# Kernel optimization log

Measured on AMD Instinct MI355X. Metric: run time of the kernel, lower is better.

Reference implementation:

```python
import math
import jax, jax.numpy as jnp
import numpy as np

B, T, D = 4, 2048, 1024
H = 16
DK = D // H


def setup_inputs() -> dict:
    key = jax.random.key(0)
    ks = jax.random.split(key, 9)
    s = 1.0 / math.sqrt(D)
    return {
        "x": jax.random.normal(ks[0], (B, T, D), dtype=jnp.float32),
        "Wq": jax.random.normal(ks[1], (D, D), dtype=jnp.float32) * s,
        "bq": jax.random.normal(ks[2], (D,), dtype=jnp.float32) * s,
        "Wk": jax.random.normal(ks[3], (D, D), dtype=jnp.float32) * s,
        "bk": jax.random.normal(ks[4], (D,), dtype=jnp.float32) * s,
        "Wv": jax.random.normal(ks[5], (D, D), dtype=jnp.float32) * s,
        "bv": jax.random.normal(ks[6], (D,), dtype=jnp.float32) * s,
        "Wo": jax.random.normal(ks[7], (D, D), dtype=jnp.float32) * s,
        "bo": jax.random.normal(ks[8], (D,), dtype=jnp.float32) * s,
    }


def reference(x, Wq, bq, Wk, bk, Wv, bv, Wo, bo):
    Bx, Tx, C = x.shape
    # projections -> [B, H, T, d_k]
    q = (x @ Wq + bq).reshape(Bx, Tx, H, DK).transpose(0, 2, 1, 3)
    k = (x @ Wk + bk).reshape(Bx, Tx, H, DK).transpose(0, 2, 1, 3)
    v = (x @ Wv + bv).reshape(Bx, Tx, H, DK).transpose(0, 2, 1, 3)
    # scores [B, H, T, T], scaled
    scores = jnp.einsum("bhqd,bhkd->bhqk", q, k) / math.sqrt(DK)
    causal = jnp.tril(jnp.ones((Tx, Tx), dtype=bool))
    scores = jnp.where(causal[None, None, :, :], scores, -jnp.inf)
    attn = jax.nn.softmax(scores, axis=-1)  # dropout p=0.0 (eval)
    out = jnp.einsum("bhqk,bhkd->bhqd", attn, v)
    out = out.transpose(0, 2, 1, 3).reshape(Bx, Tx, C)
    return out @ Wo + bo
```

## Files before the change

kernel.cpp:

```cpp
#include <hip/hip_runtime.h>
#include <stdint.h>
#include <math.h>

typedef __attribute__((ext_vector_type(8))) __bf16 bf16x8;
typedef __attribute__((ext_vector_type(4))) __bf16 bf16x4;
typedef __attribute__((ext_vector_type(4))) float f32x4;
typedef __attribute__((ext_vector_type(4))) short short4v;

__device__ __forceinline__ void load_lds16(const void* g, void* l) {
  __builtin_amdgcn_global_load_lds((__attribute__((address_space(1))) void*)(g),
                                   (__attribute__((address_space(3))) void*)(l),
                                   16, 0, 0);
}

__device__ __forceinline__ uint32_t pack_bf2(float a, float b) {
  union { __bf16 h; uint16_t u; } x, y;
  x.h = (__bf16)a; y.h = (__bf16)b;
  return (uint32_t)x.u | ((uint32_t)y.u << 16);
}

__device__ __forceinline__ short4v mk4(uint32_t lo, uint32_t hi) {
  union { uint32_t d[2]; short4v v; } u;
  u.d[0] = lo; u.d[1] = hi;
  return u.v;
}

__device__ __forceinline__ f32x4 mfma16(short4v a, short4v b, f32x4 c) {
#if defined(__has_builtin) && __has_builtin(__builtin_amdgcn_mfma_f32_16x16x16bf16_1k)
  return __builtin_amdgcn_mfma_f32_16x16x16bf16_1k(a, b, c, 0, 0, 0);
#else
  asm volatile("v_mfma_f32_16x16x16_bf16 %0, %1, %2, %0"
               : "+v"(c) : "v"(a), "v"(b));
  return c;
#endif
}

__global__ __launch_bounds__(256)
void convert_x(const float* __restrict__ xf, __bf16* __restrict__ xb) {
  const size_t i = ((size_t)blockIdx.x * 256 + threadIdx.x) * 8;
  const float4 u0 = *(const float4*)(xf + i);
  const float4 u1 = *(const float4*)(xf + i + 4);
  bf16x8 v;
  v[0] = (__bf16)u0.x; v[1] = (__bf16)u0.y; v[2] = (__bf16)u0.z; v[3] = (__bf16)u0.w;
  v[4] = (__bf16)u1.x; v[5] = (__bf16)u1.y; v[6] = (__bf16)u1.z; v[7] = (__bf16)u1.w;
  *(bf16x8*)&xb[i] = v;
}

__global__ __launch_bounds__(256)
void prep_weights(const float* __restrict__ Wq, const float* __restrict__ Wk,
                  const float* __restrict__ Wv, const float* __restrict__ Wo,
                  const float* __restrict__ bq, const float* __restrict__ bk,
                  const float* __restrict__ bv, const float* __restrict__ bo,
                  __bf16* __restrict__ Bt1, __bf16* __restrict__ Bt2,
                  float* __restrict__ bqkv, float* __restrict__ bo_f) {
  const int m = blockIdx.z;
  const float* W = (m == 0) ? Wq : (m == 1) ? Wk : (m == 2) ? Wv : Wo;
  __bf16* Out = (m == 3) ? Bt2 : Bt1 + (size_t)m * 1024 * 1024;
  const int kt = blockIdx.x * 64, nt = blockIdx.y * 64;
  __shared__ __bf16 tile[64 * 68];
  const int t = threadIdx.x;
#pragma unroll
  for (int i = 0; i < 16; i++) {
    int e = i * 256 + t;
    int r = e >> 6, c = e & 63;
    tile[r * 68 + c] = (__bf16)W[(size_t)(kt + r) * 1024 + nt + c];
  }
  __syncthreads();
#pragma unroll
  for (int i = 0; i < 16; i++) {
    int e = i * 256 + t;
    int r = e >> 6, c = e & 63;
    Out[(size_t)(nt + r) * 1024 + kt + c] = tile[c * 68 + r];
  }
  if (blockIdx.x == 0 && blockIdx.y == 0) {
    if (m < 3) {
      const float* bsrc = (m == 0) ? bq : (m == 1) ? bk : bv;
      for (int i = t; i < 1024; i += 256) bqkv[m * 1024 + i] = bsrc[i];
    } else {
      for (int i = t; i < 1024; i += 256) bo_f[i] = bo[i];
    }
  }
}

__global__ __launch_bounds__(256)
void gemm_bt(const __bf16* __restrict__ A, const __bf16* __restrict__ Bt,
             const float* __restrict__ bias, void* __restrict__ Cv,
             int out_f32, int M, int N, int K) {
  __shared__ __align__(16) __bf16 As[128 * 32];
  __shared__ __align__(16) __bf16 Bs[128 * 32];
  const int t = threadIdx.x;
  const int lane = t & 63;
  const int wave = t >> 6;
  const int bm = blockIdx.x * 128;
  const int bn = blockIdx.y * 128;
  const int wm = (wave >> 1) * 64;
  const int wn = (wave & 1) * 64;
  const int fm = lane & 15, fk = (lane >> 4) * 8;
  f32x4 acc[4][4] = {};

  const int r0 = t >> 2, kc = (t & 3) * 8;
  const __bf16* Ag0 = A + (size_t)(bm + r0) * K + kc;
  const __bf16* Ag1 = A + (size_t)(bm + 64 + r0) * K + kc;
  const __bf16* Bg0 = Bt + (size_t)(bn + r0) * K + kc;
  const __bf16* Bg1 = Bt + (size_t)(bn + 64 + r0) * K + kc;

  for (int k0 = 0; k0 < K; k0 += 32) {
    load_lds16(Ag0 + k0, &As[t * 8]);
    load_lds16(Ag1 + k0, &As[2048 + t * 8]);
    load_lds16(Bg0 + k0, &Bs[t * 8]);
    load_lds16(Bg1 + k0, &Bs[2048 + t * 8]);
    asm volatile("s_waitcnt vmcnt(0)" ::: "memory");
    __syncthreads();
    bf16x8 af[4], bfr[4];
#pragma unroll
    for (int i = 0; i < 4; i++) {
      af[i] = *(const bf16x8*)&As[(wm + i * 16 + fm) * 32 + fk];
      bfr[i] = *(const bf16x8*)&Bs[(wn + i * 16 + fm) * 32 + fk];
    }
#pragma unroll
    for (int i = 0; i < 4; i++)
#pragma unroll
      for (int j = 0; j < 4; j++)
        acc[i][j] = __builtin_amdgcn_mfma_f32_16x16x32_bf16(af[i], bfr[j], acc[i][j], 0, 0, 0);
    __syncthreads();
  }

  const int cm = (lane >> 4) * 4, cn = lane & 15;
#pragma unroll
  for (int i = 0; i < 4; i++)
#pragma unroll
    for (int j = 0; j < 4; j++) {
      const int col = bn + wn + j * 16 + cn;
      const float bvv = bias[col];
#pragma unroll
      for (int r = 0; r < 4; r++) {
        const int row = bm + wm + i * 16 + cm + r;
        const float val = acc[i][j][r] + bvv;
        if (out_f32) ((float*)Cv)[(size_t)row * N + col] = val;
        else ((__bf16*)Cv)[(size_t)row * N + col] = (__bf16)val;
      }
    }
}

__global__ __launch_bounds__(256)
void transpose_v(const __bf16* __restrict__ QKV, __bf16* __restrict__ Vt) {
  const int tt = blockIdx.x;
  const int bh = blockIdx.y;
  const int b = bh >> 4, h = bh & 15;
  __shared__ __bf16 tile[64 * 68];
  const int t = threadIdx.x;
#pragma unroll
  for (int i = 0; i < 16; i++) {
    int e = i * 256 + t;
    int tok = e >> 6, dk = e & 63;
    tile[tok * 68 + dk] =
        QKV[((size_t)b * 2048 + tt * 64 + tok) * 3072 + 2048 + h * 64 + dk];
  }
  __syncthreads();
#pragma unroll
  for (int i = 0; i < 16; i++) {
    int e = i * 256 + t;
    int dk = e >> 6, tok = e & 63;
    Vt[((size_t)bh * 64 + dk) * 2048 + tt * 64 + tok] = tile[tok * 68 + dk];
  }
}

__global__ __launch_bounds__(256)
void flash_attn(const __bf16* __restrict__ QKV, const __bf16* __restrict__ Vt,
                __bf16* __restrict__ O) {
  const int y = blockIdx.y;
  const int g = y >> 2, iy = y & 3;
  const int qt = (g == 0) ? (15 - iy)
               : (g == 1) ? iy
               : (g == 2) ? (7 - iy)
                          : (8 + iy);
  const int bh = blockIdx.x;
  const int b = bh >> 4, h = bh & 15;
  __shared__ __align__(16) __bf16 Ks[2][64 * 64];
  __shared__ __align__(16) __bf16 Vs[2][64 * 64];
  const int t = threadIdx.x, lane = t & 63, wave = t >> 6;
  const int fm = lane & 15, fq = lane >> 4;
  const int tok0 = t >> 3;
  const int csw = ((t & 7) ^ (tok0 & 7)) << 3;
  const int swb = (fm & 7) << 4;
  const int rb0 = (((fq << 4)) ^ swb) >> 1;
  const int rb1 = ((64 + (fq << 4)) ^ swb) >> 1;
  int voff[4];
#pragma unroll
  for (int nt = 0; nt < 4; nt++)
    voff[nt] = (((((nt << 1) | (fq >> 1))) ^ (fm & 7)) << 3) | ((fq & 1) << 2);

  const size_t kbase = ((size_t)b * 2048) * 3072 + 1024 + h * 64;
  const size_t vbase = (size_t)bh * 64 * 2048;
  const int nkt = 2 * qt + 2;
  const int qw = qt * 128 + wave * 32;
  const int qmax_w = qw + 31;
  const float SC = 0.18033688011112042f;
  const float THR_RAW = 44.3614195558365f;

  bf16x8 qf[2][2];
#pragma unroll
  for (int mi = 0; mi < 2; mi++) {
    const size_t qrow = ((size_t)b * 2048 + qw + mi * 16 + fm) * 3072 + h * 64;
    qf[mi][0] = *(const bf16x8*)&QKV[qrow + fq * 8];
    qf[mi][1] = *(const bf16x8*)&QKV[qrow + 32 + fq * 8];
  }

  const short4v ones4 = {(short)0x3F80, (short)0x3F80, (short)0x3F80, (short)0x3F80};

  f32x4 o_acc[2][4] = {};
  float m_i[2] = {-1e30f, -1e30f}, l_i[2] = {0.f, 0.f};

#define STAGE(KT, BUF)                                                          \
  {                                                                             \
    const int kb2 = (KT) * 64;                                                  \
    load_lds16(&QKV[kbase + (size_t)(kb2 + tok0) * 3072 + csw],                 \
               &Ks[BUF][t * 8]);                                                \
    load_lds16(&QKV[kbase + (size_t)(kb2 + 32 + tok0) * 3072 + csw],            \
               &Ks[BUF][2048 + t * 8]);                                         \
    load_lds16(&Vt[vbase + (size_t)tok0 * 2048 + kb2 + csw],                    \
               &Vs[BUF][t * 8]);                                                \
    load_lds16(&Vt[vbase + (size_t)(tok0 + 32) * 2048 + kb2 + csw],             \
               &Vs[BUF][2048 + t * 8]);                                         \
  }

  STAGE(0, 0);
  __syncthreads();
  int cur = 0;

  for (int kt = 0; kt < nkt; kt++) {
    const int kb = kt * 64;
    if (kt + 1 < nkt) STAGE(kt + 1, cur ^ 1);

    if (kb <= qmax_w) {
      const __bf16* Kc = Ks[cur];
      const __bf16* Vc = Vs[cur];

      f32x4 s[2][4];
      __builtin_amdgcn_s_setprio(1);
#pragma unroll
      for (int nt = 0; nt < 4; nt++) {
        const bf16x8 kf0 = *(const bf16x8*)&Kc[(nt * 16 + fm) * 64 + rb0];
        const bf16x8 kf1 = *(const bf16x8*)&Kc[(nt * 16 + fm) * 64 + rb1];
#pragma unroll
        for (int mi = 0; mi < 2; mi++) {
          f32x4 z = {};
          z = __builtin_amdgcn_mfma_f32_16x16x32_bf16(kf0, qf[mi][0], z, 0, 0, 0);
          z = __builtin_amdgcn_mfma_f32_16x16x32_bf16(kf1, qf[mi][1], z, 0, 0, 0);
          s[mi][nt] = z;
        }
      }
      __builtin_amdgcn_s_setprio(0);

      if (kb + 63 > qw) {
#pragma unroll
        for (int mi = 0; mi < 2; mi++) {
          const int qq = qw + mi * 16 + fm;
#pragma unroll
          for (int nt = 0; nt < 4; nt++) {
            const int kk = kb + nt * 16 + fq * 4;
#pragma unroll
            for (int r = 0; r < 4; r++)
              if (kk + r > qq) s[mi][nt][r] = -1e30f;
          }
        }
      }

      float rmax[2];
#pragma unroll
      for (int mi = 0; mi < 2; mi++) {
        float a = fmaxf(fmaxf(s[mi][0][0], s[mi][0][1]),
                        fmaxf(s[mi][0][2], s[mi][0][3]));
#pragma unroll
        for (int nt = 1; nt < 4; nt++)
          a = fmaxf(a, fmaxf(fmaxf(s[mi][nt][0], s[mi][nt][1]),
                             fmaxf(s[mi][nt][2], s[mi][nt][3])));
        a = fmaxf(a, __shfl_xor(a, 16, 64));
        a = fmaxf(a, __shfl_xor(a, 32, 64));
        rmax[mi] = a;
      }

      const float grow = fmaxf(rmax[0] - m_i[0], rmax[1] - m_i[1]);
      if (!__all(grow <= THR_RAW)) {
#pragma unroll
        for (int mi = 0; mi < 2; mi++) {
          const float mn = fmaxf(m_i[mi], rmax[mi]);
          const float a = exp2f(SC * (m_i[mi] - mn));
          m_i[mi] = mn;
          l_i[mi] *= a;
#pragma unroll
          for (int dt = 0; dt < 4; dt++)
#pragma unroll
            for (int r = 0; r < 4; r++) o_acc[mi][dt][r] *= a;
        }
      }

      short4v pb[2][4];
#pragma unroll
      for (int mi = 0; mi < 2; mi++) {
        const float msc = -SC * m_i[mi];
#pragma unroll
        for (int nt = 0; nt < 4; nt++) {
          const float p0 = exp2f(fmaf(s[mi][nt][0], SC, msc));
          const float p1 = exp2f(fmaf(s[mi][nt][1], SC, msc));
          const float p2 = exp2f(fmaf(s[mi][nt][2], SC, msc));
          const float p3 = exp2f(fmaf(s[mi][nt][3], SC, msc));
          pb[mi][nt] = mk4(pack_bf2(p0, p1), pack_bf2(p2, p3));
        }
      }

      f32x4 rsv[2];
#pragma unroll
      for (int mi = 0; mi < 2; mi++) {
        f32x4 rs = {};
#pragma unroll
        for (int nt = 0; nt < 4; nt++) rs = mfma16(ones4, pb[mi][nt], rs);
        rsv[mi] = rs;
      }

      __builtin_amdgcn_s_setprio(1);
#pragma unroll
      for (int dt = 0; dt < 4; dt++) {
        const int rowb = (dt * 16 + fm) * 64;
        short4v vf[4];
#pragma unroll
        for (int nt = 0; nt < 4; nt++)
          vf[nt] = *(const short4v*)&Vc[rowb + voff[nt]];
#pragma unroll
        for (int mi = 0; mi < 2; mi++) {
          f32x4 o = o_acc[mi][dt];
#pragma unroll
          for (int nt = 0; nt < 4; nt++) o = mfma16(vf[nt], pb[mi][nt], o);
          o_acc[mi][dt] = o;
        }
      }
      __builtin_amdgcn_s_setprio(0);

#pragma unroll
      for (int mi = 0; mi < 2; mi++) l_i[mi] += rsv[mi][0];
    }

    __syncthreads();
    cur ^= 1;
  }

#pragma unroll
  for (int mi = 0; mi < 2; mi++) {
    const float linv = 1.f / l_i[mi];
    const size_t orow = (size_t)b * 2048 + qw + mi * 16 + fm;
#pragma unroll
    for (int dt = 0; dt < 4; dt++) {
      bf16x4 w;
#pragma unroll
      for (int r = 0; r < 4; r++) w[r] = (__bf16)(o_acc[mi][dt][r] * linv);
      *(bf16x4*)&O[orow * 1024 + h * 64 + dt * 16 + fq * 4] = w;
    }
  }
#undef STAGE
}

extern "C" void kernel_launch(void* const* d_in, const int* in_sizes, int n_in,
                              void* d_out, int out_size, void* d_ws, size_t ws_size,
                              hipStream_t stream) {
  const float* x = (const float*)d_in[0];
  const float* Wq = (const float*)d_in[1];
  const float* bq = (const float*)d_in[2];
  const float* Wk = (const float*)d_in[3];
  const float* bk = (const float*)d_in[4];
  const float* Wv = (const float*)d_in[5];
  const float* bv = (const float*)d_in[6];
  const float* Wo = (const float*)d_in[7];
  const float* bo = (const float*)d_in[8];

  char* ws = (char*)d_ws;
  __bf16* Bt1 = (__bf16*)(ws);
  __bf16* Bt2 = (__bf16*)(ws + 6291456);
  float* bqkv = (float*)(ws + 8388608);
  float* bo_f = (float*)(ws + 8400896);
  __bf16* QKV = (__bf16*)(ws + 8405504);
  __bf16* Vt = (__bf16*)(ws + 58737152);
  __bf16* Xb = (__bf16*)(ws + 75514368);
  __bf16* Ow = Xb;

  hipLaunchKernelGGL(convert_x, dim3(4096), dim3(256), 0, stream, x, Xb);
  hipLaunchKernelGGL(prep_weights, dim3(16, 16, 4), dim3(256), 0, stream,
                     Wq, Wk, Wv, Wo, bq, bk, bv, bo, Bt1, Bt2, bqkv, bo_f);
  hipLaunchKernelGGL(gemm_bt, dim3(64, 24), dim3(256), 0, stream,
                     Xb, Bt1, bqkv, (void*)QKV, 0, 8192, 3072, 1024);
  hipLaunchKernelGGL(transpose_v, dim3(32, 64), dim3(256), 0, stream, QKV, Vt);
  hipLaunchKernelGGL(flash_attn, dim3(64, 16), dim3(256), 0, stream, QKV, Vt, Ow);
  hipLaunchKernelGGL(gemm_bt, dim3(64, 8), dim3(256), 0, stream,
                     Ow, Bt2, bo_f, d_out, 1, 8192, 1024, 1024);
}
```

Baseline: 329.1 us.

## Pair high and low causal query tiles per 512-thread flash attention block

Each flash-attention block now runs 8 waves and handles two query tiles, a late one (15-p) and an early one (p). Every wave takes 16 rows from each tile, so K/V staged into LDS is shared by both tiles and the causal work is balanced across blocks. The grid halves to 64x8, and each thread issues half as many LDS staging loads. The tradeoff is more divergent per-tile branching, serialised per-tile softmax/PV work, V fragments reloaded once per tile, and bigger blocks that may lower occupancy.

```diff
diff --git a/kernel.cpp b/kernel.cpp
--- a/kernel.cpp
+++ b/kernel.cpp
@@ -165,15 +165,12 @@
   }
 }
 
-__global__ __launch_bounds__(256)
+__global__ __launch_bounds__(512)
 void flash_attn(const __bf16* __restrict__ QKV, const __bf16* __restrict__ Vt,
                 __bf16* __restrict__ O) {
   const int y = blockIdx.y;
-  const int g = y >> 2, iy = y & 3;
-  const int qt = (g == 0) ? (15 - iy)
-               : (g == 1) ? iy
-               : (g == 2) ? (7 - iy)
-                          : (8 + iy);
+  const int p = (y < 4) ? y : 11 - y;
+  const int qhi = 15 - p, qlo = p;
   const int bh = blockIdx.x;
   const int b = bh >> 4, h = bh & 15;
   __shared__ __align__(16) __bf16 Ks[2][64 * 64];
@@ -192,16 +189,15 @@
 
   const size_t kbase = ((size_t)b * 2048) * 3072 + 1024 + h * 64;
   const size_t vbase = (size_t)bh * 64 * 2048;
-  const int nkt = 2 * qt + 2;
-  const int qw = qt * 128 + wave * 32;
-  const int qmax_w = qw + 31;
+  const int nkt = 2 * qhi + 2;
+  const int qmin[2] = {qhi * 128 + wave * 16, qlo * 128 + wave * 16};
   const float SC = 0.18033688011112042f;
   const float THR_RAW = 44.3614195558365f;
 
   bf16x8 qf[2][2];
 #pragma unroll
   for (int mi = 0; mi < 2; mi++) {
-    const size_t qrow = ((size_t)b * 2048 + qw + mi * 16 + fm) * 3072 + h * 64;
+    const size_t qrow = ((size_t)b * 2048 + qmin[mi] + fm) * 3072 + h * 64;
     qf[mi][0] = *(const bf16x8*)&QKV[qrow + fq * 8];
     qf[mi][1] = *(const bf16x8*)&QKV[qrow + 32 + fq * 8];
   }
@@ -216,12 +212,8 @@
     const int kb2 = (KT) * 64;                                                  \
     load_lds16(&QKV[kbase + (size_t)(kb2 + tok0) * 3072 + csw],                 \
                &Ks[BUF][t * 8]);                                                \
-    load_lds16(&QKV[kbase + (size_t)(kb2 + 32 + tok0) * 3072 + csw],            \
-               &Ks[BUF][2048 + t * 8]);                                         \
     load_lds16(&Vt[vbase + (size_t)tok0 * 2048 + kb2 + csw],                    \
                &Vs[BUF][t * 8]);                                                \
-    load_lds16(&Vt[vbase + (size_t)(tok0 + 32) * 2048 + kb2 + csw],             \
-               &Vs[BUF][2048 + t * 8]);                                         \
   }
 
   STAGE(0, 0);
@@ -232,7 +224,9 @@
     const int kb = kt * 64;
     if (kt + 1 < nkt) STAGE(kt + 1, cur ^ 1);
 
-    if (kb <= qmax_w) {
+    const bool act0 = (kb <= qmin[0] + 15);
+    const bool act1 = (kb <= qmin[1] + 15);
+    if (act0) {
       const __bf16* Kc = Ks[cur];
       const __bf16* Vc = Vs[cur];
 
@@ -242,20 +236,26 @@
       for (int nt = 0; nt < 4; nt++) {
         const bf16x8 kf0 = *(const bf16x8*)&Kc[(nt * 16 + fm) * 64 + rb0];
         const bf16x8 kf1 = *(const bf16x8*)&Kc[(nt * 16 + fm) * 64 + rb1];
-#pragma unroll
-        for (int mi = 0; mi < 2; mi++) {
+        {
           f32x4 z = {};
-          z = __builtin_amdgcn_mfma_f32_16x16x32_bf16(kf0, qf[mi][0], z, 0, 0, 0);
-          z = __builtin_amdgcn_mfma_f32_16x16x32_bf16(kf1, qf[mi][1], z, 0, 0, 0);
-          s[mi][nt] = z;
+          z = __builtin_amdgcn_mfma_f32_16x16x32_bf16(kf0, qf[0][0], z, 0, 0, 0);
+          z = __builtin_amdgcn_mfma_f32_16x16x32_bf16(kf1, qf[0][1], z, 0, 0, 0);
+          s[0][nt] = z;
+        }
+        if (act1) {
+          f32x4 z = {};
+          z = __builtin_amdgcn_mfma_f32_16x16x32_bf16(kf0, qf[1][0], z, 0, 0, 0);
+          z = __builtin_amdgcn_mfma_f32_16x16x32_bf16(kf1, qf[1][1], z, 0, 0, 0);
+          s[1][nt] = z;
         }
       }
       __builtin_amdgcn_s_setprio(0);
 
-      if (kb + 63 > qw) {
-#pragma unroll
-        for (int mi = 0; mi < 2; mi++) {
-          const int qq = qw + mi * 16 + fm;
+#pragma unroll
+      for (int mi = 0; mi < 2; mi++) {
+        if (mi == 1 && !act1) continue;
+        if (kb + 63 > qmin[mi]) {
+          const int qq = qmin[mi] + fm;
 #pragma unroll
           for (int nt = 0; nt < 4; nt++) {
             const int kk = kb + nt * 16 + fq * 4;
@@ -266,9 +266,10 @@
         }
       }
 
-      float rmax[2];
 #pragma unroll
       for (int mi = 0; mi < 2; mi++) {
+        if (mi == 1 && !act1) continue;
+
         float a = fmaxf(fmaxf(s[mi][0][0], s[mi][0][1]),
                         fmaxf(s[mi][0][2], s[mi][0][3]));
 #pragma unroll
@@ -277,27 +278,20 @@
                              fmaxf(s[mi][nt][2], s[mi][nt][3])));
         a = fmaxf(a, __shfl_xor(a, 16, 64));
         a = fmaxf(a, __shfl_xor(a, 32, 64));
-        rmax[mi] = a;
-      }
-
-      const float grow = fmaxf(rmax[0] - m_i[0], rmax[1] - m_i[1]);
-      if (!__all(grow <= THR_RAW)) {
-#pragma unroll
-        for (int mi = 0; mi < 2; mi++) {
-          const float mn = fmaxf(m_i[mi], rmax[mi]);
-          const float a = exp2f(SC * (m_i[mi] - mn));
+        const float rmax = a;
+
+        if (!__all(rmax - m_i[mi] <= THR_RAW)) {
+          const float mn = fmaxf(m_i[mi], rmax);
+          const float al = exp2f(SC * (m_i[mi] - mn));
           m_i[mi] = mn;
-          l_i[mi] *= a;
+          l_i[mi] *= al;
 #pragma unroll
           for (int dt = 0; dt < 4; dt++)
 #pragma unroll
-            for (int r = 0; r < 4; r++) o_acc[mi][dt][r] *= a;
-        }
-      }
-
-      short4v pb[2][4];
-#pragma unroll
-      for (int mi = 0; mi < 2; mi++) {
+            for (int r = 0; r < 4; r++) o_acc[mi][dt][r] *= al;
+        }
+
+        short4v pb[4];
         const float msc = -SC * m_i[mi];
 #pragma unroll
         for (int nt = 0; nt < 4; nt++) {
@@ -305,39 +299,29 @@
           const float p1 = exp2f(fmaf(s[mi][nt][1], SC, msc));
           const float p2 = exp2f(fmaf(s[mi][nt][2], SC, msc));
           const float p3 = exp2f(fmaf(s[mi][nt][3], SC, msc));
-          pb[mi][nt] = mk4(pack_bf2(p0, p1), pack_bf2(p2, p3));
-        }
+          pb[nt] = mk4(pack_bf2(p0, p1), pack_bf2(p2, p3));
+        }
+
+        f32x4 rs = {};
+#pragma unroll
+        for (int nt = 0; nt < 4; nt++) rs = mfma16(ones4, pb[nt], rs);
+
+        __builtin_amdgcn_s_setprio(1);
+#pragma unroll
+        for (int dt = 0; dt < 4; dt++) {
+          const int rowb = (dt * 16 + fm) * 64;
+          f32x4 o = o_acc[mi][dt];
+#pragma unroll
+          for (int nt = 0; nt < 4; nt++) {
+            const short4v vf = *(const short4v*)&Vc[rowb + voff[nt]];
+            o = mfma16(vf, pb[nt], o);
+          }
+          o_acc[mi][dt] = o;
+        }
+        __builtin_amdgcn_s_setprio(0);
+
+        l_i[mi] += rs[0];
       }
-
-      f32x4 rsv[2];
-#pragma unroll
-      for (int mi = 0; mi < 2; mi++) {
-        f32x4 rs = {};
-#pragma unroll
-        for (int nt = 0; nt < 4; nt++) rs = mfma16(ones4, pb[mi][nt], rs);
-        rsv[mi] = rs;
-      }
-
-      __builtin_amdgcn_s_setprio(1);
-#pragma unroll
-      for (int dt = 0; dt < 4; dt++) {
-        const int rowb = (dt * 16 + fm) * 64;
-        short4v vf[4];
-#pragma unroll
-        for (int nt = 0; nt < 4; nt++)
-          vf[nt] = *(const short4v*)&Vc[rowb + voff[nt]];
-#pragma unroll
-        for (int mi = 0; mi < 2; mi++) {
-          f32x4 o = o_acc[mi][dt];
-#pragma unroll
-          for (int nt = 0; nt < 4; nt++) o = mfma16(vf[nt], pb[mi][nt], o);
-          o_acc[mi][dt] = o;
-        }
-      }
-      __builtin_amdgcn_s_setprio(0);
-
-#pragma unroll
-      for (int mi = 0; mi < 2; mi++) l_i[mi] += rsv[mi][0];
     }
 
     __syncthreads();
@@ -347,7 +331,7 @@
 #pragma unroll
   for (int mi = 0; mi < 2; mi++) {
     const float linv = 1.f / l_i[mi];
-    const size_t orow = (size_t)b * 2048 + qw + mi * 16 + fm;
+    const size_t orow = (size_t)b * 2048 + qmin[mi] + fm;
 #pragma unroll
     for (int dt = 0; dt < 4; dt++) {
       bf16x4 w;
@@ -388,7 +372,7 @@
   hipLaunchKernelGGL(gemm_bt, dim3(64, 24), dim3(256), 0, stream,
                      Xb, Bt1, bqkv, (void*)QKV, 0, 8192, 3072, 1024);
   hipLaunchKernelGGL(transpose_v, dim3(32, 64), dim3(256), 0, stream, QKV, Vt);
-  hipLaunchKernelGGL(flash_attn, dim3(64, 16), dim3(256), 0, stream, QKV, Vt, Ow);
+  hipLaunchKernelGGL(flash_attn, dim3(64, 8), dim3(512), 0, stream, QKV, Vt, Ow);
   hipLaunchKernelGGL(gemm_bt, dim3(64, 8), dim3(256), 0, stream,
                      Ow, Bt2, bo_f, d_out, 1, 8192, 1024, 1024);
 }
```

After: 318.6 us. -3.2%, faster.
